# Performance work log

Hardware: AMD Instinct MI355X
Metric: run time of the kernel (lower is better)

## Reference

```python
import jax, jax.numpy as jnp
import numpy as np

K = 20           # top_k
EPS_NORM = 1e-12  # F.normalize default eps


def setup_inputs() -> dict:
    key = jax.random.key(0)
    ks = jax.random.split(key, 16)
    B, C, R, S, SCB, ST, H = 8192, 3755, 214, 13, 30, 6, 64
    return {
        "char_logits": jax.random.normal(ks[0], (B, C), jnp.float32),
        "radical_logits": jax.random.normal(ks[1], (B, R), jnp.float32),
        "structure": jax.random.normal(ks[2], (B, S), jnp.float32),
        "stroke_count": jax.random.normal(ks[3], (B, SCB), jnp.float32),
        "stroke_types": jax.random.normal(ks[4], (B, ST), jnp.float32),
        "radical_mask": jax.random.randint(ks[5], (C, R), 0, 2, jnp.int32),
        "structure_label": jax.random.randint(ks[6], (C,), 0, S, jnp.int32),
        "stroke_count_label": jax.random.randint(ks[7], (C,), 0, SCB, jnp.int32),
        "stroke_type_sig": jax.random.uniform(ks[8], (C, ST), jnp.float32),
        "W1": jax.random.normal(ks[9], (6, H), jnp.float32) * 0.3,
        "b1": jax.random.normal(ks[10], (H,), jnp.float32) * 0.1,
        "W2": jax.random.normal(ks[11], (H, 1), jnp.float32) * 0.3,
        "b2": jax.random.normal(ks[12], (1,), jnp.float32) * 0.1,
        "reranker_weight": jnp.asarray(0.1, jnp.float32),
    }


def _features(char_logits, radical_logits, structure, stroke_count, stroke_types,
              radical_mask, structure_label, stroke_count_label, stroke_type_sig,
              top_idx):
    sg = jax.lax.stop_gradient
    # all model outputs except char_logits are detached by caller; char_logits
    # is detached inside _compute_features for the neural-confidence feature
    rl, st, sc, sty = sg(radical_logits), sg(structure), sg(stroke_count), sg(stroke_types)
    cl_d = sg(char_logits)

    # feature 1/2: radical match & false-alarm ratios
    radical_probs = jax.nn.sigmoid(rl)                              # (B, R)
    cand_mask = radical_mask[top_idx].astype(jnp.float32)           # (B, K, R)
    detected = jnp.einsum('br,bkr->bk', radical_probs, cand_mask)   # (B, K)
    cand_counts = jnp.maximum(cand_mask.sum(-1), 1.0)
    radical_match_ratio = detected / cand_counts
    total_prob = jnp.maximum(radical_probs.sum(-1, keepdims=True), 1e-6)  # (B,1)
    false_alarm_mass = radical_probs.sum(-1, keepdims=True) - detected
    radical_false_ratio = false_alarm_mass / total_prob

    # feature 3: structure match probability
    structure_probs = jax.nn.softmax(st, axis=-1)                   # (B, S)
    cand_structure = structure_label[top_idx]                       # (B, K)
    structure_match = jnp.take_along_axis(structure_probs, cand_structure, axis=1)

    # feature 4: normalized stroke-count distance
    stroke_pred = jnp.argmax(sc, axis=-1)                           # (B,)
    cand_stroke = stroke_count_label[top_idx]                       # (B, K)
    stroke_distance = jnp.abs(stroke_pred[:, None] - cand_stroke).astype(jnp.float32) / 29.0

    # feature 5: zero-masked stroke-type cosine
    cand_sig = stroke_type_sig[top_idx]                             # (B, K, 6)
    sig_norm_val = jnp.linalg.norm(cand_sig, axis=-1)               # (B, K)
    has_sig = (sig_norm_val > 1e-6).astype(jnp.float32)
    pred_norm = sty / jnp.maximum(jnp.linalg.norm(sty, axis=-1, keepdims=True), EPS_NORM)
    cand_adj = cand_sig + 1e-8 * (1.0 - has_sig)[..., None]
    cand_norm = cand_adj / jnp.maximum(jnp.linalg.norm(cand_adj, axis=-1, keepdims=True), EPS_NORM)
    stroke_type_cos = jnp.einsum('bd,bkd->bk', pred_norm, cand_norm) * has_sig

    # feature 6: detached neural confidence
    neural_probs = jax.nn.softmax(cl_d, axis=-1)                    # (B, C)
    neural_conf = jnp.take_along_axis(neural_probs, top_idx, axis=1)

    return jnp.stack([radical_match_ratio, radical_false_ratio, structure_match,
                      stroke_distance, stroke_type_cos, neural_conf], axis=-1)  # (B, K, 6)


def reference(char_logits, radical_logits, structure, stroke_count, stroke_types,
              radical_mask, structure_label, stroke_count_label, stroke_type_sig,
              W1, b1, W2, b2, reranker_weight):
    B = char_logits.shape[0]
    top_logits, top_idx = jax.lax.top_k(char_logits, K)             # (B, K)
    feats = _features(char_logits, radical_logits, structure, stroke_count,
                      stroke_types, radical_mask, structure_label,
                      stroke_count_label, stroke_type_sig, top_idx)
    h = jax.nn.relu(feats @ W1 + b1)                                # (B, K, H)
    rerank_scores = (h @ W2 + b2)[..., 0]                           # (B, K)
    combined_top = top_logits + reranker_weight * rerank_scores
    rows = jnp.arange(B)[:, None]
    return char_logits.at[rows, top_idx].set(combined_top)
```

## Files before the change

kernel.cpp:

```cpp
#include <hip/hip_runtime.h>
#include <math.h>

#define NB   8192
#define NC   3755
#define NR   214
#define NS   13
#define NSC  30
#define NST  6
#define NH   64
#define KTOP 20
#define RPB  4
#define NT   (RPB * 64)
#define NQT  15
#define NBIN 1024
#define CAP  192

__device__ __forceinline__ unsigned sortkey(float x) {
    unsigned u = __float_as_uint(x);
    return (u & 0x80000000u) ? ~u : (u | 0x80000000u);
}

__global__ __launch_bounds__(NT, 8) void reranker_kernel(
    const float* __restrict__ char_logits,
    const float* __restrict__ radical_logits,
    const float* __restrict__ structure,
    const float* __restrict__ stroke_count,
    const float* __restrict__ stroke_types,
    const int*   __restrict__ radical_mask,
    const int*   __restrict__ structure_label,
    const int*   __restrict__ stroke_count_label,
    const float* __restrict__ stroke_type_sig,
    const float* __restrict__ W1,
    const float* __restrict__ b1,
    const float* __restrict__ W2,
    const float* __restrict__ b2,
    const float* __restrict__ rw,
    float*       __restrict__ out)
{
    const int tid  = threadIdx.x;
    const int lane = tid & 63;
    const int wave = tid >> 6;
    const int row  = blockIdx.x * RPB + wave;

    __shared__ unsigned s_hist32[RPB / 2][NBIN];
    __shared__ float s_candv[RPB][CAP];
    __shared__ int   s_candi[RPB][CAP];
    __shared__ float s_probs[RPB][216];
    __shared__ float s_topv[RPB][KTOP];
    __shared__ int   s_topi[RPB][KTOP];
    __shared__ float s_struct[RPB][NS];
    __shared__ float s_aux[RPB][8];
    __shared__ int   s_cnt[RPB];
    __shared__ int   s_need[RPB];

    const int      hw  = wave >> 1;
    const unsigned hsh = (wave & 1) * 16;

    const size_t rowOff = (size_t)row * NC;
    const float* __restrict__ rin  = char_logits + rowOff;
    float*       __restrict__ rout = out + rowOff;

    const int a     = (int)((4 - (rowOff & 3)) & 3);
    const int nq    = (NC - a) >> 2;
    const int ntail = NC - a - 4 * nq;

    int ext_idx = -1;
    if (lane < a)                           ext_idx = lane;
    else if (lane >= 8 && lane < 8 + ntail) ext_idx = a + 4 * nq + (lane - 8);

    for (int i = tid; i < (RPB / 2) * NBIN; i += NT)
        (&s_hist32[0][0])[i] = 0u;
    if (tid < RPB) s_cnt[tid] = 0;

    float psum = 0.f;
#pragma unroll
    for (int i = 0; i < 4; ++i) {
        int r = lane + i * 64;
        if (r < NR) {
            float x = radical_logits[(size_t)row * NR + r];
            float pp = 1.f / (1.f + __expf(-x));
            s_probs[wave][r] = pp;
            psum += pp;
        }
    }

    if (lane == 0) {
        float sv[NS]; float m = -INFINITY;
#pragma unroll
        for (int i = 0; i < NS; ++i) { sv[i] = structure[(size_t)row * NS + i]; m = fmaxf(m, sv[i]); }
        float s = 0.f;
#pragma unroll
        for (int i = 0; i < NS; ++i) { sv[i] = __expf(sv[i] - m); s += sv[i]; }
        float inv = 1.f / s;
#pragma unroll
        for (int i = 0; i < NS; ++i) s_struct[wave][i] = sv[i] * inv;
    } else if (lane == 1) {
        float bv = -INFINITY; int bi = 0;
#pragma unroll
        for (int i = 0; i < NSC; ++i) {
            float x = stroke_count[(size_t)row * NSC + i];
            if (x > bv) { bv = x; bi = i; }
        }
        s_aux[wave][6] = (float)bi;
    } else if (lane == 2) {
        float t6[NST]; float ss = 0.f;
#pragma unroll
        for (int i = 0; i < NST; ++i) { t6[i] = stroke_types[(size_t)row * NST + i]; ss += t6[i] * t6[i]; }
        float inv = 1.f / fmaxf(sqrtf(ss), 1e-12f);
#pragma unroll
        for (int i = 0; i < NST; ++i) s_aux[wave][i] = t6[i] * inv;
    }
    __syncthreads();

    const unsigned floork1 = 0xBF800000u;
    float m0 = -INFINITY, m1 = -INFINITY, m2 = -INFINITY, m3 = -INFINITY;
    float ext = -INFINITY;
    if (ext_idx >= 0) {
        ext = rin[ext_idx]; rout[ext_idx] = ext;
        unsigned k = sortkey(ext);
        if (k >= floork1) atomicAdd(&s_hist32[hw][k >> 22], 1u << hsh);
    }
    for (int t = 0; t < NQT; ++t) {
        int q = lane + t * 64;
        if (q < nq) {
            float4 x = *reinterpret_cast<const float4*>(rin + a + 4 * q);
            *reinterpret_cast<float4*>(rout + a + 4 * q) = x;
            m0 = fmaxf(m0, x.x); m1 = fmaxf(m1, x.y);
            m2 = fmaxf(m2, x.z); m3 = fmaxf(m3, x.w);
            unsigned k0 = sortkey(x.x), k1 = sortkey(x.y);
            unsigned k2 = sortkey(x.z), k3 = sortkey(x.w);
            if (k0 >= floork1) atomicAdd(&s_hist32[hw][k0 >> 22], 1u << hsh);
            if (k1 >= floork1) atomicAdd(&s_hist32[hw][k1 >> 22], 1u << hsh);
            if (k2 >= floork1) atomicAdd(&s_hist32[hw][k2 >> 22], 1u << hsh);
            if (k3 >= floork1) atomicAdd(&s_hist32[hw][k3 >> 22], 1u << hsh);
        }
    }
    float lmax = fmaxf(fmaxf(m0, m1), fmaxf(fmaxf(m2, m3), ext));
#pragma unroll
    for (int off = 32; off > 0; off >>= 1) lmax = fmaxf(lmax, __shfl_xor(lmax, off));
    const float rowmax = lmax;
    __syncthreads();

    int B0 = -1;
    {
        int bb = (int)(sortkey(rowmax) >> 22);
        int fb = (int)(floork1 >> 22);
        int cum = 0;
        while (bb >= fb) {
            cum += (int)((s_hist32[hw][bb] >> hsh) & 0xFFFFu);
            if (cum >= KTOP) break;
            --bb;
        }
        B0 = (cum >= KTOP) ? bb : -1;
    }
    const int need2 = (B0 < 0) ? 1 : 0;
    if (lane == 0) s_need[wave] = need2;
    __syncthreads();

    const int any2 = s_need[0] | s_need[1] | s_need[2] | s_need[3];
    if (any2) {
        if (need2) {
#pragma unroll
            for (int i = 0; i < NBIN / 64; ++i) s_hist32[hw][lane + i * 64] = 0u;
        }
        __syncthreads();
        if (need2) {
            for (int t = 0; t < NQT; ++t) {
                int q = lane + t * 64;
                if (q < nq) {
                    float4 x = *reinterpret_cast<const float4*>(rin + a + 4 * q);
                    atomicAdd(&s_hist32[hw][sortkey(x.x) >> 22], 1u << hsh);
                    atomicAdd(&s_hist32[hw][sortkey(x.y) >> 22], 1u << hsh);
                    atomicAdd(&s_hist32[hw][sortkey(x.z) >> 22], 1u << hsh);
                    atomicAdd(&s_hist32[hw][sortkey(x.w) >> 22], 1u << hsh);
                }
            }
            if (ext_idx >= 0) atomicAdd(&s_hist32[hw][sortkey(ext) >> 22], 1u << hsh);
        }
        __syncthreads();
        if (need2) {
            int bb = (int)(sortkey(rowmax) >> 22);
            int cum = 0;
            while (bb >= 0) {
                cum += (int)((s_hist32[hw][bb] >> hsh) & 0xFFFFu);
                if (cum >= KTOP) break;
                --bb;
            }
            B0 = bb;
        }
    }

    float e0 = 0.f, e1 = 0.f, e2 = 0.f, e3 = 0.f;
    if (ext_idx >= 0) {
        e0 = __expf(ext - rowmax);
        if ((int)(sortkey(ext) >> 22) >= B0) {
            int pos = atomicAdd(&s_cnt[wave], 1);
            if (pos < CAP) { s_candv[wave][pos] = ext; s_candi[wave][pos] = ext_idx; }
        }
    }
    for (int t = 0; t < NQT; ++t) {
        int q = lane + t * 64;
        if (q < nq) {
            float4 x = *reinterpret_cast<const float4*>(rin + a + 4 * q);
            e0 += __expf(x.x - rowmax);
            e1 += __expf(x.y - rowmax);
            e2 += __expf(x.z - rowmax);
            e3 += __expf(x.w - rowmax);
            if ((int)(sortkey(x.x) >> 22) >= B0) {
                int pos = atomicAdd(&s_cnt[wave], 1);
                if (pos < CAP) { s_candv[wave][pos] = x.x; s_candi[wave][pos] = a + 4*q + 0; }
            }
            if ((int)(sortkey(x.y) >> 22) >= B0) {
                int pos = atomicAdd(&s_cnt[wave], 1);
                if (pos < CAP) { s_candv[wave][pos] = x.y; s_candi[wave][pos] = a + 4*q + 1; }
            }
            if ((int)(sortkey(x.z) >> 22) >= B0) {
                int pos = atomicAdd(&s_cnt[wave], 1);
                if (pos < CAP) { s_candv[wave][pos] = x.z; s_candi[wave][pos] = a + 4*q + 2; }
            }
            if ((int)(sortkey(x.w) >> 22) >= B0) {
                int pos = atomicAdd(&s_cnt[wave], 1);
                if (pos < CAP) { s_candv[wave][pos] = x.w; s_candi[wave][pos] = a + 4*q + 3; }
            }
        }
    }
    float le = (e0 + e1) + (e2 + e3);
#pragma unroll
    for (int off = 32; off > 0; off >>= 1) le += __shfl_xor(le, off);
    const float sumexp = le;
#pragma unroll
    for (int off = 32; off > 0; off >>= 1) psum += __shfl_xor(psum, off);
    const float total = psum;
    __syncthreads();

    int M = s_cnt[wave]; if (M > CAP) M = CAP;

    for (int c = lane; c < M; c += 64) {
        float cv = s_candv[wave][c]; int ci = s_candi[wave][c];
        int rank = 0;
        for (int j = 0; j < M; ++j) {
            float ov = s_candv[wave][j]; int oi = s_candi[wave][j];
            rank += (ov > cv || (ov == cv && oi < ci)) ? 1 : 0;
        }
        if (rank < KTOP) { s_topv[wave][rank] = cv; s_topi[wave][rank] = ci; }
    }
    __syncthreads();

    const float b1v = b1[lane];
    float w1v[6];
#pragma unroll
    for (int j = 0; j < 6; ++j) w1v[j] = W1[j * NH + lane];
    const float w2v = W2[lane];
    const float b2v = b2[0];
    const float wrk = rw[0];
    const float spred = s_aux[wave][6];

    for (int k = 0; k < KTOP; ++k) {
        const int   ci = __builtin_amdgcn_readfirstlane(s_topi[wave][k]);
        const float tv = s_topv[wave][k];
        const int* __restrict__ mrow = radical_mask + (size_t)ci * NR;
        float det = 0.f, cnt = 0.f;
#pragma unroll
        for (int i = 0; i < 4; ++i) {
            int r = lane + i * 64;
            if (r < NR) {
                float m = (float)mrow[r];
                det += s_probs[wave][r] * m;
                cnt += m;
            }
        }
#pragma unroll
        for (int off = 32; off > 0; off >>= 1) {
            det += __shfl_xor(det, off);
            cnt += __shfl_xor(cnt, off);
        }
        float f1 = det / fmaxf(cnt, 1.f);
        float f2 = (total - det) / fmaxf(total, 1e-6f);
        float f3 = s_struct[wave][structure_label[ci]];
        float f4 = fabsf(spred - (float)stroke_count_label[ci]) * (1.f / 29.f);
        float sig[NST]; float ss = 0.f;
#pragma unroll
        for (int i = 0; i < NST; ++i) { sig[i] = stroke_type_sig[(size_t)ci * NST + i]; ss += sig[i] * sig[i]; }
        float nrm = sqrtf(ss);
        float has = (nrm > 1e-6f) ? 1.f : 0.f;
        float add = 1e-8f * (1.f - has);
        float ss2 = 0.f;
#pragma unroll
        for (int i = 0; i < NST; ++i) { sig[i] += add; ss2 += sig[i] * sig[i]; }
        float inv = 1.f / fmaxf(sqrtf(ss2), 1e-12f);
        float dot = 0.f;
#pragma unroll
        for (int i = 0; i < NST; ++i) dot += s_aux[wave][i] * sig[i] * inv;
        float f5 = dot * has;
        float f6 = __expf(tv - rowmax) / sumexp;

        float acc = b1v + f1 * w1v[0] + f2 * w1v[1] + f3 * w1v[2]
                        + f4 * w1v[3] + f5 * w1v[4] + f6 * w1v[5];
        float h = fmaxf(acc, 0.f);
        float part = h * w2v;
#pragma unroll
        for (int off = 32; off > 0; off >>= 1) part += __shfl_xor(part, off);
        if (lane == 0) rout[ci] = tv + wrk * (part + b2v);
    }
}

extern "C" void kernel_launch(void* const* d_in, const int* in_sizes, int n_in,
                              void* d_out, int out_size, void* d_ws, size_t ws_size,
                              hipStream_t stream) {
    (void)in_sizes; (void)n_in; (void)out_size; (void)d_ws; (void)ws_size;
    const float* char_logits        = (const float*)d_in[0];
    const float* radical_logits     = (const float*)d_in[1];
    const float* structure          = (const float*)d_in[2];
    const float* stroke_count      = (const float*)d_in[3];
    const float* stroke_types       = (const float*)d_in[4];
    const int*   radical_mask       = (const int*)d_in[5];
    const int*   structure_label    = (const int*)d_in[6];
    const int*   stroke_count_label = (const int*)d_in[7];
    const float* stroke_type_sig    = (const float*)d_in[8];
    const float* W1                 = (const float*)d_in[9];
    const float* b1                 = (const float*)d_in[10];
    const float* W2                 = (const float*)d_in[11];
    const float* b2                 = (const float*)d_in[12];
    const float* rw                 = (const float*)d_in[13];
    float* out = (float*)d_out;

    reranker_kernel<<<NB / RPB, NT, 0, stream>>>(
        char_logits, radical_logits, structure, stroke_count, stroke_types,
        radical_mask, structure_label, stroke_count_label, stroke_type_sig,
        W1, b1, W2, b2, rw, out);
}
```

Measured before the change: 405.7 us.

## Split fused reranker into top-k select kernel and per-row rerank kernel

Splits the single fused kernel into two. The first handles the char_logits copy, histogram-based top-k selection and softmax statistics, and writes the top-k and row stats to workspace. The second uses one 256-thread block per row, spreading the 20 candidate feature/MLP evaluations over 4 waves instead of running them serially in one wave. The histogram prefilter floor rises to -2.0, and candidates are packed as 64-bit keys so ranking needs one comparison. The aim is a lighter register/LDS footprint in the streaming pass and more parallelism in the latency-bound rerank tail, at the cost of a second launch and a workspace round trip.

```diff
diff --git a/kernel.cpp b/kernel.cpp
--- a/kernel.cpp
+++ b/kernel.cpp
@@ -19,9 +19,179 @@
     unsigned u = __float_as_uint(x);
     return (u & 0x80000000u) ? ~u : (u | 0x80000000u);
 }
-
-__global__ __launch_bounds__(NT, 8) void reranker_kernel(
+__device__ __forceinline__ float inv_sortkey(unsigned k) {
+    unsigned u = (k & 0x80000000u) ? (k ^ 0x80000000u) : ~k;
+    return __uint_as_float(u);
+}
+
+__global__ __launch_bounds__(NT, 8) void select_kernel(
     const float* __restrict__ char_logits,
+    float*       __restrict__ out,
+    float*       __restrict__ ws_topv,
+    int*         __restrict__ ws_topi,
+    float*       __restrict__ ws_stat)
+{
+    const int tid  = threadIdx.x;
+    const int lane = tid & 63;
+    const int wave = tid >> 6;
+    const int row  = blockIdx.x * RPB + wave;
+
+    __shared__ unsigned           s_hist32[RPB / 2][NBIN];
+    __shared__ unsigned long long s_cand[RPB][CAP];
+    __shared__ int s_cnt[RPB];
+    __shared__ int s_need[RPB];
+
+    const int      hw  = wave >> 1;
+    const unsigned hsh = (wave & 1) * 16;
+
+    const size_t rowOff = (size_t)row * NC;
+    const float* __restrict__ rin  = char_logits + rowOff;
+    float*       __restrict__ rout = out + rowOff;
+
+    const int a     = (int)((4 - (rowOff & 3)) & 3);
+    const int nq    = (NC - a) >> 2;
+    const int ntail = NC - a - 4 * nq;
+
+    int ext_idx = -1;
+    if (lane < a)                           ext_idx = lane;
+    else if (lane >= 8 && lane < 8 + ntail) ext_idx = a + 4 * nq + (lane - 8);
+
+    for (int i = tid; i < (RPB / 2) * NBIN; i += NT)
+        (&s_hist32[0][0])[i] = 0u;
+    if (tid < RPB) s_cnt[tid] = 0;
+    __syncthreads();
+
+    const unsigned floork1 = 0xC0000000u;
+    float m0 = -INFINITY, m1 = -INFINITY, m2 = -INFINITY, m3 = -INFINITY;
+    float ext = -INFINITY;
+    if (ext_idx >= 0) {
+        ext = rin[ext_idx]; rout[ext_idx] = ext;
+        unsigned k = sortkey(ext);
+        if (k >= floork1) atomicAdd(&s_hist32[hw][k >> 22], 1u << hsh);
+    }
+    for (int t = 0; t < NQT; ++t) {
+        int q = lane + t * 64;
+        if (q < nq) {
+            float4 x = *reinterpret_cast<const float4*>(rin + a + 4 * q);
+            *reinterpret_cast<float4*>(rout + a + 4 * q) = x;
+            m0 = fmaxf(m0, x.x); m1 = fmaxf(m1, x.y);
+            m2 = fmaxf(m2, x.z); m3 = fmaxf(m3, x.w);
+            unsigned k0 = sortkey(x.x), k1 = sortkey(x.y);
+            unsigned k2 = sortkey(x.z), k3 = sortkey(x.w);
+            if (k0 >= floork1) atomicAdd(&s_hist32[hw][k0 >> 22], 1u << hsh);
+            if (k1 >= floork1) atomicAdd(&s_hist32[hw][k1 >> 22], 1u << hsh);
+            if (k2 >= floork1) atomicAdd(&s_hist32[hw][k2 >> 22], 1u << hsh);
+            if (k3 >= floork1) atomicAdd(&s_hist32[hw][k3 >> 22], 1u << hsh);
+        }
+    }
+    float lmax = fmaxf(fmaxf(m0, m1), fmaxf(fmaxf(m2, m3), ext));
+#pragma unroll
+    for (int off = 32; off > 0; off >>= 1) lmax = fmaxf(lmax, __shfl_xor(lmax, off));
+    const float rowmax = lmax;
+    __syncthreads();
+
+    int B0 = -1;
+    {
+        int bb = (int)(sortkey(rowmax) >> 22);
+        int fb = (int)(floork1 >> 22);
+        int cum = 0;
+        while (bb >= fb) {
+            cum += (int)((s_hist32[hw][bb] >> hsh) & 0xFFFFu);
+            if (cum >= KTOP) break;
+            --bb;
+        }
+        B0 = (cum >= KTOP) ? bb : -1;
+    }
+    const int need2 = (B0 < 0) ? 1 : 0;
+    if (lane == 0) s_need[wave] = need2;
+    __syncthreads();
+
+    const int any2 = s_need[0] | s_need[1] | s_need[2] | s_need[3];
+    if (any2) {
+        if (need2) {
+#pragma unroll
+            for (int i = 0; i < NBIN / 64; ++i) s_hist32[hw][lane + i * 64] = 0u;
+        }
+        __syncthreads();
+        if (need2) {
+            for (int t = 0; t < NQT; ++t) {
+                int q = lane + t * 64;
+                if (q < nq) {
+                    float4 x = *reinterpret_cast<const float4*>(rin + a + 4 * q);
+                    atomicAdd(&s_hist32[hw][sortkey(x.x) >> 22], 1u << hsh);
+                    atomicAdd(&s_hist32[hw][sortkey(x.y) >> 22], 1u << hsh);
+                    atomicAdd(&s_hist32[hw][sortkey(x.z) >> 22], 1u << hsh);
+                    atomicAdd(&s_hist32[hw][sortkey(x.w) >> 22], 1u << hsh);
+                }
+            }
+            if (ext_idx >= 0) atomicAdd(&s_hist32[hw][sortkey(ext) >> 22], 1u << hsh);
+        }
+        __syncthreads();
+        if (need2) {
+            int bb = (int)(sortkey(rowmax) >> 22);
+            int cum = 0;
+            while (bb >= 0) {
+                cum += (int)((s_hist32[hw][bb] >> hsh) & 0xFFFFu);
+                if (cum >= KTOP) break;
+                --bb;
+            }
+            B0 = bb;
+        }
+    }
+
+    float e0 = 0.f, e1 = 0.f, e2 = 0.f, e3 = 0.f;
+    if (ext_idx >= 0) {
+        e0 = __expf(ext - rowmax);
+        unsigned k = sortkey(ext);
+        if ((int)(k >> 22) >= B0) {
+            int pos = atomicAdd(&s_cnt[wave], 1);
+            if (pos < CAP)
+                s_cand[wave][pos] = ((unsigned long long)k << 32) | (0xFFFFFFFFu - (unsigned)ext_idx);
+        }
+    }
+    for (int t = 0; t < NQT; ++t) {
+        int q = lane + t * 64;
+        if (q < nq) {
+            float4 x = *reinterpret_cast<const float4*>(rin + a + 4 * q);
+            e0 += __expf(x.x - rowmax);
+            e1 += __expf(x.y - rowmax);
+            e2 += __expf(x.z - rowmax);
+            e3 += __expf(x.w - rowmax);
+            unsigned kk[4] = { sortkey(x.x), sortkey(x.y), sortkey(x.z), sortkey(x.w) };
+#pragma unroll
+            for (int j = 0; j < 4; ++j) {
+                if ((int)(kk[j] >> 22) >= B0) {
+                    int pos = atomicAdd(&s_cnt[wave], 1);
+                    if (pos < CAP)
+                        s_cand[wave][pos] = ((unsigned long long)kk[j] << 32)
+                                          | (0xFFFFFFFFu - (unsigned)(a + 4*q + j));
+                }
+            }
+        }
+    }
+    float le = (e0 + e1) + (e2 + e3);
+#pragma unroll
+    for (int off = 32; off > 0; off >>= 1) le += __shfl_xor(le, off);
+    __syncthreads();
+
+    int M = s_cnt[wave]; if (M > CAP) M = CAP;
+
+    for (int c = lane; c < M; c += 64) {
+        unsigned long long pc = s_cand[wave][c];
+        int rank = 0;
+        for (int j = 0; j < M; ++j) rank += (s_cand[wave][j] > pc) ? 1 : 0;
+        if (rank < KTOP) {
+            ws_topv[(size_t)row * KTOP + rank] = inv_sortkey((unsigned)(pc >> 32));
+            ws_topi[(size_t)row * KTOP + rank] = (int)(0xFFFFFFFFu - (unsigned)(pc & 0xFFFFFFFFu));
+        }
+    }
+    if (lane == 0) {
+        ws_stat[2 * row + 0] = rowmax;
+        ws_stat[2 * row + 1] = le;
+    }
+}
+
+__global__ __launch_bounds__(256, 8) void rerank_kernel(
     const float* __restrict__ radical_logits,
     const float* __restrict__ structure,
     const float* __restrict__ stroke_count,
@@ -35,56 +205,30 @@
     const float* __restrict__ W2,
     const float* __restrict__ b2,
     const float* __restrict__ rw,
+    const float* __restrict__ ws_topv,
+    const int*   __restrict__ ws_topi,
+    const float* __restrict__ ws_stat,
     float*       __restrict__ out)
 {
+    const int row  = blockIdx.x;
     const int tid  = threadIdx.x;
     const int lane = tid & 63;
     const int wave = tid >> 6;
-    const int row  = blockIdx.x * RPB + wave;
-
-    __shared__ unsigned s_hist32[RPB / 2][NBIN];
-    __shared__ float s_candv[RPB][CAP];
-    __shared__ int   s_candi[RPB][CAP];
-    __shared__ float s_probs[RPB][216];
-    __shared__ float s_topv[RPB][KTOP];
-    __shared__ int   s_topi[RPB][KTOP];
-    __shared__ float s_struct[RPB][NS];
-    __shared__ float s_aux[RPB][8];
-    __shared__ int   s_cnt[RPB];
-    __shared__ int   s_need[RPB];
-
-    const int      hw  = wave >> 1;
-    const unsigned hsh = (wave & 1) * 16;
-
-    const size_t rowOff = (size_t)row * NC;
-    const float* __restrict__ rin  = char_logits + rowOff;
-    float*       __restrict__ rout = out + rowOff;
-
-    const int a     = (int)((4 - (rowOff & 3)) & 3);
-    const int nq    = (NC - a) >> 2;
-    const int ntail = NC - a - 4 * nq;
-
-    int ext_idx = -1;
-    if (lane < a)                           ext_idx = lane;
-    else if (lane >= 8 && lane < 8 + ntail) ext_idx = a + 4 * nq + (lane - 8);
-
-    for (int i = tid; i < (RPB / 2) * NBIN; i += NT)
-        (&s_hist32[0][0])[i] = 0u;
-    if (tid < RPB) s_cnt[tid] = 0;
-
-    float psum = 0.f;
-#pragma unroll
-    for (int i = 0; i < 4; ++i) {
-        int r = lane + i * 64;
-        if (r < NR) {
-            float x = radical_logits[(size_t)row * NR + r];
-            float pp = 1.f / (1.f + __expf(-x));
-            s_probs[wave][r] = pp;
-            psum += pp;
-        }
-    }
-
-    if (lane == 0) {
+
+    __shared__ float s_probs[216];
+    __shared__ float s_struct[NS];
+    __shared__ float s_aux[8];
+    __shared__ float s_topv[KTOP];
+    __shared__ int   s_topi[KTOP];
+    __shared__ float s_stat2[2];
+
+    if (tid < NR)
+        s_probs[tid] = 1.f / (1.f + __expf(-radical_logits[(size_t)row * NR + tid]));
+    if (tid < KTOP) {
+        s_topv[tid] = ws_topv[(size_t)row * KTOP + tid];
+        s_topi[tid] = ws_topi[(size_t)row * KTOP + tid];
+    }
+    if (tid == 216) {
         float sv[NS]; float m = -INFINITY;
 #pragma unroll
         for (int i = 0; i < NS; ++i) { sv[i] = structure[(size_t)row * NS + i]; m = fmaxf(m, sv[i]); }
@@ -93,159 +237,40 @@
         for (int i = 0; i < NS; ++i) { sv[i] = __expf(sv[i] - m); s += sv[i]; }
         float inv = 1.f / s;
 #pragma unroll
-        for (int i = 0; i < NS; ++i) s_struct[wave][i] = sv[i] * inv;
-    } else if (lane == 1) {
+        for (int i = 0; i < NS; ++i) s_struct[i] = sv[i] * inv;
+    } else if (tid == 217) {
         float bv = -INFINITY; int bi = 0;
 #pragma unroll
         for (int i = 0; i < NSC; ++i) {
             float x = stroke_count[(size_t)row * NSC + i];
             if (x > bv) { bv = x; bi = i; }
         }
-        s_aux[wave][6] = (float)bi;
-    } else if (lane == 2) {
+        s_aux[6] = (float)bi;
+    } else if (tid == 218) {
         float t6[NST]; float ss = 0.f;
 #pragma unroll
         for (int i = 0; i < NST; ++i) { t6[i] = stroke_types[(size_t)row * NST + i]; ss += t6[i] * t6[i]; }
         float inv = 1.f / fmaxf(sqrtf(ss), 1e-12f);
 #pragma unroll
-        for (int i = 0; i < NST; ++i) s_aux[wave][i] = t6[i] * inv;
-    }
-    __syncthreads();
-
-    const unsigned floork1 = 0xBF800000u;
-    float m0 = -INFINITY, m1 = -INFINITY, m2 = -INFINITY, m3 = -INFINITY;
-    float ext = -INFINITY;
-    if (ext_idx >= 0) {
-        ext = rin[ext_idx]; rout[ext_idx] = ext;
-        unsigned k = sortkey(ext);
-        if (k >= floork1) atomicAdd(&s_hist32[hw][k >> 22], 1u << hsh);
-    }
-    for (int t = 0; t < NQT; ++t) {
-        int q = lane + t * 64;
-        if (q < nq) {
-            float4 x = *reinterpret_cast<const float4*>(rin + a + 4 * q);
-            *reinterpret_cast<float4*>(rout + a + 4 * q) = x;
-            m0 = fmaxf(m0, x.x); m1 = fmaxf(m1, x.y);
-            m2 = fmaxf(m2, x.z); m3 = fmaxf(m3, x.w);
-            unsigned k0 = sortkey(x.x), k1 = sortkey(x.y);
-            unsigned k2 = sortkey(x.z), k3 = sortkey(x.w);
-            if (k0 >= floork1) atomicAdd(&s_hist32[hw][k0 >> 22], 1u << hsh);
-            if (k1 >= floork1) atomicAdd(&s_hist32[hw][k1 >> 22], 1u << hsh);
-            if (k2 >= floork1) atomicAdd(&s_hist32[hw][k2 >> 22], 1u << hsh);
-            if (k3 >= floork1) atomicAdd(&s_hist32[hw][k3 >> 22], 1u << hsh);
-        }
-    }
-    float lmax = fmaxf(fmaxf(m0, m1), fmaxf(fmaxf(m2, m3), ext));
-#pragma unroll
-    for (int off = 32; off > 0; off >>= 1) lmax = fmaxf(lmax, __shfl_xor(lmax, off));
-    const float rowmax = lmax;
-    __syncthreads();
-
-    int B0 = -1;
-    {
-        int bb = (int)(sortkey(rowmax) >> 22);
-        int fb = (int)(floork1 >> 22);
-        int cum = 0;
-        while (bb >= fb) {
-            cum += (int)((s_hist32[hw][bb] >> hsh) & 0xFFFFu);
-            if (cum >= KTOP) break;
-            --bb;
-        }
-        B0 = (cum >= KTOP) ? bb : -1;
-    }
-    const int need2 = (B0 < 0) ? 1 : 0;
-    if (lane == 0) s_need[wave] = need2;
-    __syncthreads();
-
-    const int any2 = s_need[0] | s_need[1] | s_need[2] | s_need[3];
-    if (any2) {
-        if (need2) {
-#pragma unroll
-            for (int i = 0; i < NBIN / 64; ++i) s_hist32[hw][lane + i * 64] = 0u;
-        }
-        __syncthreads();
-        if (need2) {
-            for (int t = 0; t < NQT; ++t) {
-                int q = lane + t * 64;
-                if (q < nq) {
-                    float4 x = *reinterpret_cast<const float4*>(rin + a + 4 * q);
-                    atomicAdd(&s_hist32[hw][sortkey(x.x) >> 22], 1u << hsh);
-                    atomicAdd(&s_hist32[hw][sortkey(x.y) >> 22], 1u << hsh);
-                    atomicAdd(&s_hist32[hw][sortkey(x.z) >> 22], 1u << hsh);
-                    atomicAdd(&s_hist32[hw][sortkey(x.w) >> 22], 1u << hsh);
-                }
-            }
-            if (ext_idx >= 0) atomicAdd(&s_hist32[hw][sortkey(ext) >> 22], 1u << hsh);
-        }
-        __syncthreads();
-        if (need2) {
-            int bb = (int)(sortkey(rowmax) >> 22);
-            int cum = 0;
-            while (bb >= 0) {
-                cum += (int)((s_hist32[hw][bb] >> hsh) & 0xFFFFu);
-                if (cum >= KTOP) break;
-                --bb;
-            }
-            B0 = bb;
-        }
-    }
-
-    float e0 = 0.f, e1 = 0.f, e2 = 0.f, e3 = 0.f;
-    if (ext_idx >= 0) {
-        e0 = __expf(ext - rowmax);
-        if ((int)(sortkey(ext) >> 22) >= B0) {
-            int pos = atomicAdd(&s_cnt[wave], 1);
-            if (pos < CAP) { s_candv[wave][pos] = ext; s_candi[wave][pos] = ext_idx; }
-        }
-    }
-    for (int t = 0; t < NQT; ++t) {
-        int q = lane + t * 64;
-        if (q < nq) {
-            float4 x = *reinterpret_cast<const float4*>(rin + a + 4 * q);
-            e0 += __expf(x.x - rowmax);
-            e1 += __expf(x.y - rowmax);
-            e2 += __expf(x.z - rowmax);
-            e3 += __expf(x.w - rowmax);
-            if ((int)(sortkey(x.x) >> 22) >= B0) {
-                int pos = atomicAdd(&s_cnt[wave], 1);
-                if (pos < CAP) { s_candv[wave][pos] = x.x; s_candi[wave][pos] = a + 4*q + 0; }
-            }
-            if ((int)(sortkey(x.y) >> 22) >= B0) {
-                int pos = atomicAdd(&s_cnt[wave], 1);
-                if (pos < CAP) { s_candv[wave][pos] = x.y; s_candi[wave][pos] = a + 4*q + 1; }
-            }
-            if ((int)(sortkey(x.z) >> 22) >= B0) {
-                int pos = atomicAdd(&s_cnt[wave], 1);
-                if (pos < CAP) { s_candv[wave][pos] = x.z; s_candi[wave][pos] = a + 4*q + 2; }
-            }
-            if ((int)(sortkey(x.w) >> 22) >= B0) {
-                int pos = atomicAdd(&s_cnt[wave], 1);
-                if (pos < CAP) { s_candv[wave][pos] = x.w; s_candi[wave][pos] = a + 4*q + 3; }
-            }
-        }
-    }
-    float le = (e0 + e1) + (e2 + e3);
-#pragma unroll
-    for (int off = 32; off > 0; off >>= 1) le += __shfl_xor(le, off);
-    const float sumexp = le;
+        for (int i = 0; i < NST; ++i) s_aux[i] = t6[i] * inv;
+    } else if (tid == 219) {
+        s_stat2[0] = ws_stat[2 * row + 0];
+        s_stat2[1] = ws_stat[2 * row + 1];
+    }
+    __syncthreads();
+
+    float psum = 0.f;
+#pragma unroll
+    for (int i = 0; i < 4; ++i) {
+        int r = lane + i * 64;
+        if (r < NR) psum += s_probs[r];
+    }
 #pragma unroll
     for (int off = 32; off > 0; off >>= 1) psum += __shfl_xor(psum, off);
     const float total = psum;
-    __syncthreads();
-
-    int M = s_cnt[wave]; if (M > CAP) M = CAP;
-
-    for (int c = lane; c < M; c += 64) {
-        float cv = s_candv[wave][c]; int ci = s_candi[wave][c];
-        int rank = 0;
-        for (int j = 0; j < M; ++j) {
-            float ov = s_candv[wave][j]; int oi = s_candi[wave][j];
-            rank += (ov > cv || (ov == cv && oi < ci)) ? 1 : 0;
-        }
-        if (rank < KTOP) { s_topv[wave][rank] = cv; s_topi[wave][rank] = ci; }
-    }
-    __syncthreads();
-
+
+    const float rowmax = s_stat2[0];
+    const float sumexp = s_stat2[1];
     const float b1v = b1[lane];
     float w1v[6];
 #pragma unroll
@@ -253,11 +278,13 @@
     const float w2v = W2[lane];
     const float b2v = b2[0];
     const float wrk = rw[0];
-    const float spred = s_aux[wave][6];
-
-    for (int k = 0; k < KTOP; ++k) {
-        const int   ci = __builtin_amdgcn_readfirstlane(s_topi[wave][k]);
-        const float tv = s_topv[wave][k];
+    const float spred = s_aux[6];
+
+#pragma unroll
+    for (int j = 0; j < KTOP / 4; ++j) {
+        const int   k  = wave * (KTOP / 4) + j;
+        const int   ci = __builtin_amdgcn_readfirstlane(s_topi[k]);
+        const float tv = s_topv[k];
         const int* __restrict__ mrow = radical_mask + (size_t)ci * NR;
         float det = 0.f, cnt = 0.f;
 #pragma unroll
@@ -265,7 +292,7 @@
             int r = lane + i * 64;
             if (r < NR) {
                 float m = (float)mrow[r];
-                det += s_probs[wave][r] * m;
+                det += s_probs[r] * m;
                 cnt += m;
             }
         }
@@ -276,7 +303,7 @@
         }
         float f1 = det / fmaxf(cnt, 1.f);
         float f2 = (total - det) / fmaxf(total, 1e-6f);
-        float f3 = s_struct[wave][structure_label[ci]];
+        float f3 = s_struct[structure_label[ci]];
         float f4 = fabsf(spred - (float)stroke_count_label[ci]) * (1.f / 29.f);
         float sig[NST]; float ss = 0.f;
 #pragma unroll
@@ -290,7 +317,7 @@
         float inv = 1.f / fmaxf(sqrtf(ss2), 1e-12f);
         float dot = 0.f;
 #pragma unroll
-        for (int i = 0; i < NST; ++i) dot += s_aux[wave][i] * sig[i] * inv;
+        for (int i = 0; i < NST; ++i) dot += s_aux[i] * sig[i] * inv;
         float f5 = dot * has;
         float f6 = __expf(tv - rowmax) / sumexp;
 
@@ -300,18 +327,18 @@
         float part = h * w2v;
 #pragma unroll
         for (int off = 32; off > 0; off >>= 1) part += __shfl_xor(part, off);
-        if (lane == 0) rout[ci] = tv + wrk * (part + b2v);
+        if (lane == 0) out[(size_t)row * NC + ci] = tv + wrk * (part + b2v);
     }
 }
 
 extern "C" void kernel_launch(void* const* d_in, const int* in_sizes, int n_in,
                               void* d_out, int out_size, void* d_ws, size_t ws_size,
                               hipStream_t stream) {
-    (void)in_sizes; (void)n_in; (void)out_size; (void)d_ws; (void)ws_size;
+    (void)in_sizes; (void)n_in; (void)out_size; (void)ws_size;
     const float* char_logits        = (const float*)d_in[0];
     const float* radical_logits     = (const float*)d_in[1];
     const float* structure          = (const float*)d_in[2];
-    const float* stroke_count      = (const float*)d_in[3];
+    const float* stroke_count       = (const float*)d_in[3];
     const float* stroke_types       = (const float*)d_in[4];
     const int*   radical_mask       = (const int*)d_in[5];
     const int*   structure_label    = (const int*)d_in[6];
@@ -324,8 +351,13 @@
     const float* rw                 = (const float*)d_in[13];
     float* out = (float*)d_out;
 
-    reranker_kernel<<<NB / RPB, NT, 0, stream>>>(
-        char_logits, radical_logits, structure, stroke_count, stroke_types,
+    float* ws_topv = (float*)d_ws;
+    int*   ws_topi = (int*)(ws_topv + (size_t)NB * KTOP);
+    float* ws_stat = (float*)(ws_topi + (size_t)NB * KTOP);
+
+    select_kernel<<<NB / RPB, NT, 0, stream>>>(char_logits, out, ws_topv, ws_topi, ws_stat);
+    rerank_kernel<<<NB, 256, 0, stream>>>(
+        radical_logits, structure, stroke_count, stroke_types,
         radical_mask, structure_label, stroke_count_label, stroke_type_sig,
-        W1, b1, W2, b2, rw, out);
-}
+        W1, b1, W2, b2, rw, ws_topv, ws_topi, ws_stat, out);
+}
```

Measured after the change: 391.0 us. 3.6% less time.
